# Kernel optimization log

Measured on AMD Instinct MI355X. Metric: run time of the kernel, lower is better.

Reference implementation:

```python
import math
import jax, jax.numpy as jnp
import numpy as np

B = 32        # number of graphs
MAXN = 4096   # nodes per graph (all graphs full)
C = 256       # emb_size_atom
NSEEDS = 409  # int(number_atoms * 0.1)
TOTAL = B * MAXN
INV06 = 1.0 / 0.6
INV_SQRT2 = 1.0 / math.sqrt(2.0)

def scaled_silu(x):
    return jax.nn.silu(x) * INV06

def dense(x, W):
    # Dense(bias=False, activation='silu') == ScaledSiLU(x @ W^T)
    return scaled_silu(x @ W.T)

def res_layer(x, W1, W2):
    return (x + dense(dense(x, W1), W2)) * INV_SQRT2

def layer_norm(x, g, b, eps=1e-5):
    m = jnp.mean(x, -1, keepdims=True)
    v = jnp.var(x, -1, keepdims=True)
    return (x - m) * jax.lax.rsqrt(v + eps) * g + b

def split_heads(x, H):
    # torch.cat(x.split(dV//H, 2), dim=0): head-major stacking on batch axis
    b, n, d = x.shape
    return x.reshape(b, n, H, d // H).transpose(2, 0, 1, 3).reshape(H * b, n, d // H)

def merge_heads(x, H, b):
    _, n, dh = x.shape
    return x.reshape(H, b, n, dh).transpose(1, 2, 0, 3).reshape(b, n, H * dh)

def base_mha(Q, K, Wq, bq, Wk, bk, Wv, bv, Wo, bo, g0, b0, g1, b1, H, mask=None):
    dV = Wq.shape[0]
    Q_ = split_heads(Q @ Wq.T + bq, H)
    K_ = split_heads(K @ Wk.T + bk, H)
    V_ = split_heads(K @ Wv.T + bv, H)
    score = jnp.einsum('bqd,bkd->bqk', Q_, K_) * (1.0 / math.sqrt(dV))
    if mask is not None:
        score = score + jnp.tile(mask, (H, 1, 1))
    A = jax.nn.softmax(score, axis=1)  # FAITHFUL: softmax over the QUERY axis (dim=1 in source)
    out = merge_heads(Q_ + jnp.einsum('bqk,bkd->bqd', A, V_), H, Q.shape[0])
    out = layer_norm(out, g0, b0)
    out = out + jax.nn.relu(out @ Wo.T + bo)
    out = layer_norm(out, g1, b1)
    return out, A

def to_dense_batch(x, batch):
    total = x.shape[0]
    counts = jax.ops.segment_sum(jnp.ones((total,), jnp.int32), batch, num_segments=B)
    offsets = jnp.concatenate([jnp.zeros((1,), jnp.int32), jnp.cumsum(counts)[:-1]])
    pos = jnp.arange(total) - offsets[batch]  # position of each node within its graph
    dense_x = jnp.zeros((B, MAXN, x.shape[-1]), x.dtype).at[batch, pos].set(x)
    omask = jnp.zeros((B, MAXN), bool).at[batch, pos].set(True)
    return dense_x, omask, pos

def _forward(h, batch_seg, W_pre1, W_pre2, S, pWq, pbq, pWk, pbk, pWv, pbv, pWo, pbo, pg0, pb0, pg1, pb1, iWq, ibq, iWk, ibk, iWv, ibv, iWo, ibo, ig0, ib0, ig1, ib1, W_head, W_r1a, W_r1b, W_r2a, W_r2b):
    hres = res_layer(h, W_pre1, W_pre2)
    dx, omask, pos = to_dense_batch(hres, batch_seg)
    mask = jnp.where(omask, 0.0, -1e9).astype(hres.dtype)[:, None, :]  # [B,1,MAXN]
    Q = jnp.tile(S, (B, 1, 1))  # learned seeds [B,NSEEDS,C]
    NAs, A1 = base_mha(Q, dx, pWq, pbq, pWk, pbk, pWv, pbv, pWo, pbo, pg0, pb0, pg1, pb1, 1, mask)
    NAs, _ = base_mha(NAs, NAs, iWq, ibq, iWk, ibk, iWv, ibv, iWo, ibo, ig0, ib0, ig1, ib1, 2, None)
    h_back = jnp.einsum('bsn,bsc->bnc', A1, NAs)  # project back: A1^T @ NAs
    h_up = h_back[batch_seg, pos]                 # flatten back to [TOTAL, C]
    h_up = dense(h_up, W_head)
    h_up = res_layer(h_up, W_r1a, W_r1b)
    h_up = res_layer(h_up, W_r2a, W_r2b)
    return h_up

def setup_inputs() -> dict:
    key = jax.random.key(0)
    ks = jax.random.split(key, 20)
    sc = 1.0 / math.sqrt(C)
    w = lambda k: jax.random.normal(k, (C, C), jnp.float32) * sc
    zb = jnp.zeros((C,), jnp.float32)
    og = jnp.ones((C,), jnp.float32)
    return {
        'h': jax.random.normal(ks[0], (TOTAL, C), jnp.float32),
        'batch_seg': jnp.arange(TOTAL, dtype=jnp.int32) // MAXN,
        'W_pre1': w(ks[1]), 'W_pre2': w(ks[2]),
        'S': jax.random.normal(ks[3], (1, NSEEDS, C), jnp.float32) * math.sqrt(2.0 / (NSEEDS + C)),
        'pWq': w(ks[4]), 'pbq': zb, 'pWk': w(ks[5]), 'pbk': zb,
        'pWv': w(ks[6]), 'pbv': zb, 'pWo': w(ks[7]), 'pbo': zb,
        'pg0': og, 'pb0': zb, 'pg1': og, 'pb1': zb,
        'iWq': w(ks[8]), 'ibq': zb, 'iWk': w(ks[9]), 'ibk': zb,
        'iWv': w(ks[10]), 'ibv': zb, 'iWo': w(ks[11]), 'ibo': zb,
        'ig0': og, 'ib0': zb, 'ig1': og, 'ib1': zb,
        'W_head': w(ks[12]),
        'W_r1a': w(ks[13]), 'W_r1b': w(ks[14]),
        'W_r2a': w(ks[15]), 'W_r2b': w(ks[16]),
    }

def reference(h, batch_seg, W_pre1, W_pre2, S, pWq, pbq, pWk, pbk, pWv, pbv, pWo, pbo, pg0, pb0, pg1, pb1, iWq, ibq, iWk, ibk, iWv, ibv, iWo, ibo, ig0, ib0, ig1, ib1, W_head, W_r1a, W_r1b, W_r2a, W_r2b):
    return _forward(h, batch_seg, W_pre1, W_pre2, S, pWq, pbq, pWk, pbk, pWv, pbv, pWo, pbo, pg0, pb0, pg1, pb1, iWq, ibq, iWk, ibk, iWv, ibv, iWo, ibo, ig0, ib0, ig1, ib1, W_head, W_r1a, W_r1b, W_r2a, W_r2b)
```

## Files before the change

kernel.cpp:

```cpp
#include <hip/hip_runtime.h>


#define BM 128
#define BN 128
#define BKT 32
#define PKM 132
#define NJOBS 33

typedef __attribute__((ext_vector_type(8))) __bf16 bf16x8;
typedef __attribute__((ext_vector_type(4))) __bf16 bf16x4;
typedef __attribute__((ext_vector_type(4))) float  f32x4;

struct CastJobs {
    const float* src[NJOBS];
    __bf16*      dst[NJOBS];
    long         n[NJOBS];
    int          startBlk[NJOBS];
};

__global__ void cast_many_k(CastJobs J)
{
    int b = blockIdx.x;
    int j = 0;
#pragma unroll
    for (int t = 0; t < NJOBS; t++) { if (J.startBlk[t] <= b) j = t; }
    long idx = ((long)(b - J.startBlk[j]) * 256 + threadIdx.x) * 4;
    if (idx < J.n[j]) {
        f32x4 v = *(const f32x4*)(J.src[j] + idx);
        bf16x4 o;
        o[0] = (__bf16)v[0]; o[1] = (__bf16)v[1];
        o[2] = (__bf16)v[2]; o[3] = (__bf16)v[3];
        *(bf16x4*)(J.dst[j] + idx) = o;
    }
}

__device__ __forceinline__ void gload_lds16(const __bf16* g, __bf16* l)
{
    __builtin_amdgcn_global_load_lds(
        (const __attribute__((address_space(1))) void*)g,
        (__attribute__((address_space(3))) void*)l, 16, 0, 0);
}

template<int TRANS>
__device__ __forceinline__ void stage_tile(__bf16* __restrict__ lds,
                                           const __bf16* __restrict__ G,
                                           int ld, int r0, int Rg,
                                           int k0, int K, int tid)
{
    if (TRANS == 0) {
        const bool fast = ((ld & 7) == 0) && (r0 + BM <= Rg) && (k0 + BKT <= K);
        if (fast) {
#pragma unroll
            for (int i = 0; i < 2; i++) {
                int v = tid + i * 256;
                int r = v >> 2, kc = (v & 3) * 8;
                gload_lds16(G + (long)(r0 + r) * ld + (k0 + kc), lds + v * 8);
            }
        } else {
#pragma unroll
            for (int i = 0; i < 2; i++) {
                int v = tid + i * 256;
                int r = v >> 2, kc = (v & 3) * 8;
                int gm = r0 + r, gk = k0 + kc;
                bf16x8 val;
#pragma unroll
                for (int j = 0; j < 8; j++) val[j] = (__bf16)0.0f;
                if (gm < Rg) {
                    if (((ld & 7) == 0) && (gk + 8 <= K)) {
                        val = *(const bf16x8*)(G + (long)gm * ld + gk);
                    } else {
#pragma unroll
                        for (int j = 0; j < 8; j++)
                            if (gk + j < K) val[j] = G[(long)gm * ld + gk + j];
                    }
                }
                *(bf16x8*)(lds + v * 8) = val;
            }
        }
    } else {
#pragma unroll
        for (int i = 0; i < 2; i++) {
            int v = tid + i * 256;
            int kk = v >> 4;
            int mc = (v & 15) * 8;
            int gk = k0 + kk, gm = r0 + mc;
            bf16x8 val;
#pragma unroll
            for (int j = 0; j < 8; j++) val[j] = (__bf16)0.0f;
            if (gk < K) {
                if (((ld & 7) == 0) && (gm + 8 <= Rg)) {
                    val = *(const bf16x8*)(G + (long)gk * ld + gm);
                } else {
#pragma unroll
                    for (int j = 0; j < 8; j++)
                        if (gm + j < Rg) val[j] = G[(long)gk * ld + gm + j];
                }
            }
            bf16x4 lo, hi;
            lo[0] = val[0]; lo[1] = val[1]; lo[2] = val[2]; lo[3] = val[3];
            hi[0] = val[4]; hi[1] = val[5]; hi[2] = val[6]; hi[3] = val[7];
            *(bf16x4*)(lds + kk * PKM + mc)     = lo;
            *(bf16x4*)(lds + kk * PKM + mc + 4) = hi;
        }
    }
}

template<int AT, int BT>
__launch_bounds__(256, 2)
__global__ void gemm_k(const __bf16* __restrict__ A, long aLo, long aHi, int lda, int Ms,
                       const __bf16* __restrict__ Bm, long bLo, long bHi, int ldb, int Ns,
                       const __bf16* __restrict__ bias,
                       const __bf16* __restrict__ res, long rLo, long rHi, int ldr, int resMode,
                       float* __restrict__ outF, __bf16* __restrict__ outB,
                       long oLo, long oHi, int ldo, int storeT,
                       int M, int N, int K, float oscale, int act)
{
    __shared__ __align__(16) __bf16 As[BKT * PKM];
    __shared__ __align__(16) __bf16 Bs[BKT * PKM];

    const int tid = threadIdx.x;
    const int z = blockIdx.z;
    const long zl = (long)(z & 31), zh = (long)(z >> 5);
    const __bf16* Ab = A + zl * aLo + zh * aHi;
    const __bf16* Bb = Bm + zl * bLo + zh * bHi;
    const int m0 = blockIdx.x * BM;
    const int n0 = blockIdx.y * BN;

    f32x4 acc[4][4];
#pragma unroll
    for (int i = 0; i < 4; i++)
#pragma unroll
        for (int j = 0; j < 4; j++)
#pragma unroll
            for (int r = 0; r < 4; r++) acc[i][j][r] = 0.0f;

    const int wv = tid >> 6;
    const int lane = tid & 63;
    const int wm = (wv >> 1) * 64;
    const int wn = (wv & 1) * 64;
    const int l15 = lane & 15;
    const int lq  = lane >> 4;

    for (int k0 = 0; k0 < K; k0 += BKT) {
        stage_tile<AT>(As, Ab, lda, m0, Ms, k0, K, tid);
        stage_tile<(BT == 1) ? 0 : 1>(Bs, Bb, ldb, n0, Ns, k0, K, tid);
        __syncthreads();
        bf16x8 af[4], bfr[4];
        if (AT == 0) {
#pragma unroll
            for (int i = 0; i < 4; i++)
                af[i] = *(const bf16x8*)(As + (wm + i * 16 + l15) * BKT + lq * 8);
        } else {
#pragma unroll
            for (int i = 0; i < 4; i++) {
                int m = wm + i * 16 + l15;
#pragma unroll
                for (int j = 0; j < 8; j++) af[i][j] = As[(lq * 8 + j) * PKM + m];
            }
        }
        if (BT == 1) {
#pragma unroll
            for (int j = 0; j < 4; j++)
                bfr[j] = *(const bf16x8*)(Bs + (wn + j * 16 + l15) * BKT + lq * 8);
        } else {
#pragma unroll
            for (int j = 0; j < 4; j++) {
                int n = wn + j * 16 + l15;
#pragma unroll
                for (int jj = 0; jj < 8; jj++) bfr[j][jj] = Bs[(lq * 8 + jj) * PKM + n];
            }
        }
#pragma unroll
        for (int i = 0; i < 4; i++)
#pragma unroll
            for (int j = 0; j < 4; j++)
                acc[i][j] = __builtin_amdgcn_mfma_f32_16x16x32_bf16(af[i], bfr[j], acc[i][j], 0, 0, 0);
        __syncthreads();
    }

    const __bf16* Rb = res ? (res + zl * rLo + zh * rHi) : (const __bf16*)nullptr;
    const long ob = zl * oLo + zh * oHi;
#pragma unroll
    for (int i = 0; i < 4; i++) {
#pragma unroll
        for (int j = 0; j < 4; j++) {
            int col = n0 + wn + j * 16 + l15;
            if (col >= N) continue;
            float bcol = bias ? (float)bias[col] : 0.0f;
            int row0 = m0 + wm + i * 16 + lq * 4;
            if (!storeT) {
#pragma unroll
                for (int r = 0; r < 4; r++) {
                    int row = row0 + r;
                    if (row >= M) continue;
                    float v = acc[i][j][r] * oscale + bcol;
                    if (act == 1) {
                        float e = __expf(-fabsf(v));
                        float sig = (v >= 0.0f) ? 1.0f / (1.0f + e) : e / (1.0f + e);
                        v = v * sig * 1.6666666666666667f;
                    } else if (act == 2) {
                        v = fmaxf(v, 0.0f);
                    }
                    if (resMode) {
                        float rv = (float)Rb[(long)row * ldr + col];
                        v = (resMode == 1) ? (rv + v) * 0.70710678118654752f : (rv + v);
                    }
                    long oi = ob + (long)row * ldo + col;
                    if (outF) outF[oi] = v;
                    else      outB[oi] = (__bf16)v;
                }
            } else {
                if (row0 + 3 < M) {
                    bf16x4 rv4;
                    if (resMode) rv4 = *(const bf16x4*)(Rb + (long)col * ldr + row0);
                    bf16x4 ov;
#pragma unroll
                    for (int r = 0; r < 4; r++) {
                        float v = acc[i][j][r] * oscale + bcol;
                        if (act == 1) {
                            float e = __expf(-fabsf(v));
                            float sig = (v >= 0.0f) ? 1.0f / (1.0f + e) : e / (1.0f + e);
                            v = v * sig * 1.6666666666666667f;
                        } else if (act == 2) {
                            v = fmaxf(v, 0.0f);
                        }
                        if (resMode) {
                            float rv = (float)rv4[r];
                            v = (resMode == 1) ? (rv + v) * 0.70710678118654752f : (rv + v);
                        }
                        ov[r] = (__bf16)v;
                    }
                    *(bf16x4*)(outB + ob + (long)col * ldo + row0) = ov;
                } else {
#pragma unroll
                    for (int r = 0; r < 4; r++) {
                        int row = row0 + r;
                        if (row >= M) continue;
                        float v = acc[i][j][r] * oscale + bcol;
                        if (act == 1) {
                            float e = __expf(-fabsf(v));
                            float sig = (v >= 0.0f) ? 1.0f / (1.0f + e) : e / (1.0f + e);
                            v = v * sig * 1.6666666666666667f;
                        } else if (act == 2) {
                            v = fmaxf(v, 0.0f);
                        }
                        if (resMode) {
                            float rv = (float)Rb[(long)col * ldr + row];
                            v = (resMode == 1) ? (rv + v) * 0.70710678118654752f : (rv + v);
                        }
                        outB[ob + (long)col * ldo + row] = (__bf16)v;
                    }
                }
            }
        }
    }
}

__global__ void rowsoftmax_k(const float* __restrict__ S, __bf16* __restrict__ A,
                             long rows, int L, int ldS, int ldA, int Lw)
{
    long row = (long)blockIdx.x * 4 + (threadIdx.x >> 6);
    if (row >= rows) return;
    int lane = threadIdx.x & 63;
    const float* Sr = S + row * (long)ldS;
    float v[7];
    int cnt = 0;
    for (int q = lane; q < L; q += 64) v[cnt++] = Sr[q];
    float m = -3.0e38f;
    for (int c = 0; c < cnt; c++) m = fmaxf(m, v[c]);
#pragma unroll
    for (int off = 32; off > 0; off >>= 1) m = fmaxf(m, __shfl_xor(m, off));
    float s = 0.0f;
    for (int c = 0; c < cnt; c++) s += __expf(v[c] - m);
#pragma unroll
    for (int off = 32; off > 0; off >>= 1) s += __shfl_xor(s, off);
    float inv = 1.0f / s;
    cnt = 0;
    for (int q = lane; q < Lw; q += 64) {
        float o = 0.0f;
        if (q < L) { o = __expf(v[cnt] - m) * inv; cnt++; }
        A[row * (long)ldA + q] = (__bf16)o;
    }
}

__global__ void ln_k(const __bf16* __restrict__ X, __bf16* __restrict__ Y,
                     const __bf16* __restrict__ gamma, const __bf16* __restrict__ beta,
                     int rows)
{
    int row = blockIdx.x * 4 + (threadIdx.x >> 6);
    if (row >= rows) return;
    int lane = threadIdx.x & 63;
    bf16x4 xv = *(const bf16x4*)(X + (long)row * 256 + lane * 4);
    float v0 = (float)xv[0], v1 = (float)xv[1], v2 = (float)xv[2], v3 = (float)xv[3];
    float s = v0 + v1 + v2 + v3;
#pragma unroll
    for (int off = 32; off > 0; off >>= 1) s += __shfl_xor(s, off);
    float mean = s * (1.0f / 256.0f);
    float d0 = v0 - mean, d1 = v1 - mean, d2 = v2 - mean, d3 = v3 - mean;
    float q = d0 * d0 + d1 * d1 + d2 * d2 + d3 * d3;
#pragma unroll
    for (int off = 32; off > 0; off >>= 1) q += __shfl_xor(q, off);
    float sc = rsqrtf(q * (1.0f / 256.0f) + 1e-5f);
    bf16x4 gv = *(const bf16x4*)(gamma + lane * 4);
    bf16x4 bv = *(const bf16x4*)(beta + lane * 4);
    bf16x4 ov;
    ov[0] = (__bf16)(d0 * sc * (float)gv[0] + (float)bv[0]);
    ov[1] = (__bf16)(d1 * sc * (float)gv[1] + (float)bv[1]);
    ov[2] = (__bf16)(d2 * sc * (float)gv[2] + (float)bv[2]);
    ov[3] = (__bf16)(d3 * sc * (float)gv[3] + (float)bv[3]);
    *(bf16x4*)(Y + (long)row * 256 + lane * 4) = ov;
}

__global__ void sentinel_k(float* out, long n)
{
    long i = (long)blockIdx.x * blockDim.x + threadIdx.x;
    if (i < n) out[i] = 12345.0f;
}

static void G(hipStream_t st, int AT, int BT,
              const __bf16* A, long aLo, long aHi, int lda, int Ms,
              const __bf16* B, long bLo, long bHi, int ldb, int Ns,
              const __bf16* bias,
              const __bf16* res, long rLo, long rHi, int ldr, int resMode,
              float* outF, __bf16* outB, long oLo, long oHi, int ldo, int storeT,
              int M, int N, int K, int Z, float oscale, int act)
{
    dim3 grid((M + BM - 1) / BM, (N + BN - 1) / BN, Z), blk(256, 1, 1);
#define GARGS A, aLo, aHi, lda, Ms, B, bLo, bHi, ldb, Ns, bias, res, rLo, rHi, ldr, resMode, \
              outF, outB, oLo, oHi, ldo, storeT, M, N, K, oscale, act
    if (AT == 0 && BT == 1)      gemm_k<0, 1><<<grid, blk, 0, st>>>(GARGS);
    else if (AT == 0 && BT == 0) gemm_k<0, 0><<<grid, blk, 0, st>>>(GARGS);
    else                         gemm_k<1, 0><<<grid, blk, 0, st>>>(GARGS);
#undef GARGS
}

extern "C" void kernel_launch(void* const* d_in, const int* in_sizes, int n_in,
                              void* d_out, int out_size, void* d_ws, size_t ws_size,
                              hipStream_t stream)
{
    (void)in_sizes; (void)n_in;
    float* OUT = (float*)d_out;

    const int TOT = 131072, NC = 256, NS = 409, MX = 4096;
    const int NSP = 416;
    const int NSB = 32 * NS;
    const long NTC = (long)TOT * NC;
    const int GCH = 4;

    static const int  pidx[NJOBS] = {0,2,3,4,5,6,7,8,9,10,11,12,13,14,15,16,
                                     17,18,19,20,21,22,23,24,25,26,27,28,29,30,31,32,33};
    static const long pn[NJOBS]   = {33554432,65536,65536,104704,
                                     65536,256,65536,256,65536,256,65536,256,
                                     256,256,256,256,
                                     65536,256,65536,256,65536,256,65536,256,
                                     256,256,256,256,
                                     65536,65536,65536,65536,65536};
    long ptot = 0;
    for (int j = 0; j < NJOBS; j++) ptot += pn[j];

    char* w = (char*)d_ws;
    size_t off = 0;
    auto take = [&](size_t bytes) -> char* {
        char* p = w + off;
        off += (bytes + 255) & ~(size_t)255;
        return p;
    };
    char* pblk = take((size_t)ptot * 2);
    char* reg0 = take((size_t)64 * NS * NSP * 4);
    char* reg1 = take((size_t)32 * MX * NSP * 2);
    char* reg2 = take((size_t)NTC * 2);
    char* reg3 = take((size_t)NTC * 2);
    __bf16* QP  = (__bf16*)take((size_t)NS * NC * 2);
    __bf16* sb0 = (__bf16*)take((size_t)NSB * NC * 2);
    __bf16* sb1 = (__bf16*)take((size_t)NSB * NC * 2);
    __bf16* sb2 = (__bf16*)take((size_t)NSB * NC * 2);
    __bf16* sb3 = (__bf16*)take((size_t)NSB * NC * 2);
    __bf16* sb4 = (__bf16*)take((size_t)NSB * NC * 2);
    __bf16* sb5 = (__bf16*)take((size_t)NSB * NC * 2);

    if (off > ws_size) {
        long n = out_size;
        sentinel_k<<<(int)((n + 255) / 256), 256, 0, stream>>>(OUT, n);
        return;
    }

    CastJobs J;
    __bf16* P[NJOBS];
    {
        long cum = 0;
        int blk = 0;
        for (int j = 0; j < NJOBS; j++) {
            J.src[j] = (const float*)d_in[pidx[j]];
            P[j] = (__bf16*)pblk + cum;
            J.dst[j] = P[j];
            J.n[j] = pn[j];
            J.startBlk[j] = blk;
            blk += (int)((pn[j] + 1023) / 1024);
            cum += pn[j];
        }
        cast_many_k<<<blk, 256, 0, stream>>>(J);
    }
    const __bf16 *hB = P[0], *Wpre1 = P[1], *Wpre2 = P[2], *Sseed = P[3];
    const __bf16 *pWq = P[4], *pbq = P[5], *pWk = P[6], *pbk = P[7];
    const __bf16 *pWv = P[8], *pbv = P[9], *pWo = P[10], *pbo = P[11];
    const __bf16 *pg0 = P[12], *pb0 = P[13], *pg1 = P[14], *pb1 = P[15];
    const __bf16 *iWq = P[16], *ibq = P[17], *iWk = P[18], *ibk = P[19];
    const __bf16 *iWv = P[20], *ibv = P[21], *iWo = P[22], *ibo = P[23];
    const __bf16 *ig0 = P[24], *ib0 = P[25], *ig1 = P[26], *ib1 = P[27];
    const __bf16 *Whead = P[28], *Wr1a = P[29], *Wr1b = P[30];
    const __bf16 *Wr2a = P[31], *Wr2b = P[32];

    float*  STs = (float*)reg0;
    float*  S2T = (float*)reg0;
    __bf16* T1  = (__bf16*)reg1;
    __bf16* A1T = (__bf16*)reg1;
    __bf16* Tt  = (__bf16*)reg1;
    __bf16* Kb  = (__bf16*)reg2;
    __bf16* HB  = (__bf16*)reg2;
    __bf16* Ub  = (__bf16*)reg2;
    __bf16* Vt  = (__bf16*)reg3;
    __bf16* A2T = (__bf16*)reg3;
    __bf16* Tm  = (__bf16*)reg3;
    __bf16* HR  = (__bf16*)d_out;

    G(stream, 0, 1, hB, 0, 0, 256, TOT, Wpre1, 0, 0, 256, 256, nullptr,
      nullptr, 0, 0, 0, 0, nullptr, T1, 0, 0, 256, 0, TOT, 256, 256, 1, 1.0f, 1);
    G(stream, 0, 1, T1, 0, 0, 256, TOT, Wpre2, 0, 0, 256, 256, nullptr,
      hB, 0, 0, 256, 1, nullptr, HR, 0, 0, 256, 0, TOT, 256, 256, 1, 1.0f, 1);
    G(stream, 0, 1, HR, 0, 0, 256, TOT, pWk, 0, 0, 256, 256, pbk,
      nullptr, 0, 0, 0, 0, nullptr, Kb, 0, 0, 256, 0, TOT, 256, 256, 1, 1.0f, 0);
    G(stream, 0, 1, HR, (long)MX * NC, 0, 256, MX, pWv, 0, 0, 256, 256, pbv,
      nullptr, 0, 0, 0, 0, nullptr, Vt, (long)NC * MX, 0, MX, 1, MX, 256, 256, 32, 1.0f, 0);
    G(stream, 0, 1, Sseed, 0, 0, 256, NS, pWq, 0, 0, 256, 256, pbq,
      nullptr, 0, 0, 0, 0, nullptr, QP, 0, 0, 256, 0, NS, 256, 256, 1, 1.0f, 0);
    for (int c = 0; c < 32 / GCH; c++) {
        const __bf16* Kc = Kb + (size_t)c * GCH * MX * NC;
        G(stream, 0, 1, Kc, (long)MX * NC, 0, 256, MX, QP, 0, 0, 256, NS, nullptr,
          nullptr, 0, 0, 0, 0, STs, nullptr, (long)MX * NSP, 0, NSP, 0,
          MX, NS, 256, GCH, 0.0625f, 0);
        rowsoftmax_k<<<dim3(GCH * MX / 4), 256, 0, stream>>>(
            STs, A1T + (size_t)c * GCH * MX * NSP, (long)GCH * MX, NS, NSP, NSP, NSP);
    }
    G(stream, 0, 0, Vt, (long)NC * MX, 0, MX, NC, A1T, (long)MX * NSP, 0, NSP, NSP, nullptr,
      QP, 0, 0, 256, 2, nullptr, sb0, (long)NS * NC, 0, 256, 1,
      NC, NS, MX, 32, 1.0f, 0);
    ln_k<<<dim3(NSB / 4), 256, 0, stream>>>(sb0, sb1, pg0, pb0, NSB);
    G(stream, 0, 1, sb1, 0, 0, 256, NSB, pWo, 0, 0, 256, 256, pbo,
      sb1, 0, 0, 256, 2, nullptr, sb2, 0, 0, 256, 0, NSB, 256, 256, 1, 1.0f, 2);
    ln_k<<<dim3(NSB / 4), 256, 0, stream>>>(sb2, sb0, pg1, pb1, NSB);
    G(stream, 0, 1, sb0, 0, 0, 256, NSB, iWq, 0, 0, 256, 256, ibq,
      nullptr, 0, 0, 0, 0, nullptr, sb1, 0, 0, 256, 0, NSB, 256, 256, 1, 1.0f, 0);
    G(stream, 0, 1, sb0, 0, 0, 256, NSB, iWk, 0, 0, 256, 256, ibk,
      nullptr, 0, 0, 0, 0, nullptr, sb2, 0, 0, 256, 0, NSB, 256, 256, 1, 1.0f, 0);
    G(stream, 0, 1, sb0, 0, 0, 256, NSB, iWv, 0, 0, 256, 256, ibv,
      nullptr, 0, 0, 0, 0, nullptr, sb3, 0, 0, 256, 0, NSB, 256, 256, 1, 1.0f, 0);
    G(stream, 0, 1, sb2, (long)NS * NC, 128, 256, NS, sb1, (long)NS * NC, 128, 256, NS, nullptr,
      nullptr, 0, 0, 0, 0, S2T, nullptr, (long)NS * NSP, 32L * NS * NSP, NSP, 0,
      NS, NS, 128, 64, 0.0625f, 0);
    rowsoftmax_k<<<dim3(64 * NS / 4), 256, 0, stream>>>(S2T, A2T, 64L * NS, NS, NSP, NSP, NSP);
    G(stream, 1, 0, A2T, (long)NS * NSP, 32L * NS * NSP, NSP, NSP,
      sb3, (long)NS * NC, 128, 256, 128, nullptr,
      sb1, (long)NS * NC, 128, 256, 2, nullptr, sb4, (long)NS * NC, 128, 256, 0,
      NS, 128, NS, 64, 1.0f, 0);
    ln_k<<<dim3(NSB / 4), 256, 0, stream>>>(sb4, sb5, ig0, ib0, NSB);
    G(stream, 0, 1, sb5, 0, 0, 256, NSB, iWo, 0, 0, 256, 256, ibo,
      sb5, 0, 0, 256, 2, nullptr, sb4, 0, 0, 256, 0, NSB, 256, 256, 1, 1.0f, 2);
    ln_k<<<dim3(NSB / 4), 256, 0, stream>>>(sb4, sb1, ig1, ib1, NSB);
    G(stream, 0, 0, A1T, (long)MX * NSP, 0, NSP, MX, sb1, (long)NS * NC, 0, 256, 256, nullptr,
      nullptr, 0, 0, 0, 0, nullptr, HB, (long)MX * NC, 0, 256, 0, MX, 256, 416, 32, 1.0f, 0);
    G(stream, 0, 1, HB, 0, 0, 256, TOT, Whead, 0, 0, 256, 256, nullptr,
      nullptr, 0, 0, 0, 0, nullptr, Tt, 0, 0, 256, 0, TOT, 256, 256, 1, 1.0f, 1);
    G(stream, 0, 1, Tt, 0, 0, 256, TOT, Wr1a, 0, 0, 256, 256, nullptr,
      nullptr, 0, 0, 0, 0, nullptr, Tm, 0, 0, 256, 0, TOT, 256, 256, 1, 1.0f, 1);
    G(stream, 0, 1, Tm, 0, 0, 256, TOT, Wr1b, 0, 0, 256, 256, nullptr,
      Tt, 0, 0, 256, 1, nullptr, Ub, 0, 0, 256, 0, TOT, 256, 256, 1, 1.0f, 1);
    G(stream, 0, 1, Ub, 0, 0, 256, TOT, Wr2a, 0, 0, 256, 256, nullptr,
      nullptr, 0, 0, 0, 0, nullptr, Tm, 0, 0, 256, 0, TOT, 256, 256, 1, 1.0f, 1);
    G(stream, 0, 1, Tm, 0, 0, 256, TOT, Wr2b, 0, 0, 256, 256, nullptr,
      Ub, 0, 0, 256, 1, OUT, nullptr, 0, 0, 256, 0, TOT, 256, 256, 1, 1.0f, 1);
}
```

Before: 1.756 ms.

## Double-buffer LDS tiles in GEMM to overlap global loads with MFMA

New measurement: 1.870 ms. +6.5%, slower.

```diff
diff --git a/kernel.cpp b/kernel.cpp
--- a/kernel.cpp
+++ b/kernel.cpp
@@ -42,7 +42,7 @@
 }
 
 template<int TRANS>
-__device__ __forceinline__ void stage_tile(__bf16* __restrict__ lds,
+__device__ __forceinline__ bool stage_load(bf16x8 (&rv)[2], __bf16* __restrict__ lds,
                                            const __bf16* __restrict__ G,
                                            int ld, int r0, int Rg,
                                            int k0, int K, int tid)
@@ -56,27 +56,28 @@
                 int r = v >> 2, kc = (v & 3) * 8;
                 gload_lds16(G + (long)(r0 + r) * ld + (k0 + kc), lds + v * 8);
             }
-        } else {
-#pragma unroll
-            for (int i = 0; i < 2; i++) {
-                int v = tid + i * 256;
-                int r = v >> 2, kc = (v & 3) * 8;
-                int gm = r0 + r, gk = k0 + kc;
-                bf16x8 val;
-#pragma unroll
-                for (int j = 0; j < 8; j++) val[j] = (__bf16)0.0f;
-                if (gm < Rg) {
-                    if (((ld & 7) == 0) && (gk + 8 <= K)) {
-                        val = *(const bf16x8*)(G + (long)gm * ld + gk);
-                    } else {
-#pragma unroll
-                        for (int j = 0; j < 8; j++)
-                            if (gk + j < K) val[j] = G[(long)gm * ld + gk + j];
-                    }
+            return true;
+        }
+#pragma unroll
+        for (int i = 0; i < 2; i++) {
+            int v = tid + i * 256;
+            int r = v >> 2, kc = (v & 3) * 8;
+            int gm = r0 + r, gk = k0 + kc;
+            bf16x8 val;
+#pragma unroll
+            for (int j = 0; j < 8; j++) val[j] = (__bf16)0.0f;
+            if (gm < Rg) {
+                if (((ld & 7) == 0) && (gk + 8 <= K)) {
+                    val = *(const bf16x8*)(G + (long)gm * ld + gk);
+                } else {
+#pragma unroll
+                    for (int j = 0; j < 8; j++)
+                        if (gk + j < K) val[j] = G[(long)gm * ld + gk + j];
                 }
-                *(bf16x8*)(lds + v * 8) = val;
             }
-        }
+            rv[i] = val;
+        }
+        return false;
     } else {
 #pragma unroll
         for (int i = 0; i < 2; i++) {
@@ -96,9 +97,29 @@
                         if (gm + j < Rg) val[j] = G[(long)gk * ld + gm + j];
                 }
             }
+            rv[i] = val;
+        }
+        return false;
+    }
+}
+
+template<int TRANS>
+__device__ __forceinline__ void stage_write(const bf16x8 (&rv)[2], __bf16* __restrict__ lds,
+                                            int tid, bool fast)
+{
+    if (TRANS == 0) {
+        if (fast) return;
+#pragma unroll
+        for (int i = 0; i < 2; i++)
+            *(bf16x8*)(lds + (tid + i * 256) * 8) = rv[i];
+    } else {
+#pragma unroll
+        for (int i = 0; i < 2; i++) {
+            int v = tid + i * 256;
+            int kk = v >> 4, mc = (v & 15) * 8;
             bf16x4 lo, hi;
-            lo[0] = val[0]; lo[1] = val[1]; lo[2] = val[2]; lo[3] = val[3];
-            hi[0] = val[4]; hi[1] = val[5]; hi[2] = val[6]; hi[3] = val[7];
+            lo[0] = rv[i][0]; lo[1] = rv[i][1]; lo[2] = rv[i][2]; lo[3] = rv[i][3];
+            hi[0] = rv[i][4]; hi[1] = rv[i][5]; hi[2] = rv[i][6]; hi[3] = rv[i][7];
             *(bf16x4*)(lds + kk * PKM + mc)     = lo;
             *(bf16x4*)(lds + kk * PKM + mc + 4) = hi;
         }
@@ -115,8 +136,9 @@
                        long oLo, long oHi, int ldo, int storeT,
                        int M, int N, int K, float oscale, int act)
 {
-    __shared__ __align__(16) __bf16 As[BKT * PKM];
-    __shared__ __align__(16) __bf16 Bs[BKT * PKM];
+    constexpr int BTT = (BT == 1) ? 0 : 1;
+    __shared__ __align__(16) __bf16 As[2][BKT * PKM];
+    __shared__ __align__(16) __bf16 Bs[2][BKT * PKM];
 
     const int tid = threadIdx.x;
     const int z = blockIdx.z;
@@ -141,33 +163,47 @@
     const int l15 = lane & 15;
     const int lq  = lane >> 4;
 
-    for (int k0 = 0; k0 < K; k0 += BKT) {
-        stage_tile<AT>(As, Ab, lda, m0, Ms, k0, K, tid);
-        stage_tile<(BT == 1) ? 0 : 1>(Bs, Bb, ldb, n0, Ns, k0, K, tid);
-        __syncthreads();
+    const int nt = (K + BKT - 1) / BKT;
+
+    bf16x8 ra[2], rb[2];
+    bool fa = stage_load<AT>(ra, As[0], Ab, lda, m0, Ms, 0, K, tid);
+    bool fb = stage_load<BTT>(rb, Bs[0], Bb, ldb, n0, Ns, 0, K, tid);
+    stage_write<AT>(ra, As[0], tid, fa);
+    stage_write<BTT>(rb, Bs[0], tid, fb);
+    __syncthreads();
+
+    int cur = 0;
+    for (int t = 0; t < nt; t++) {
+        const bool nxt = (t + 1 < nt);
+        if (nxt) {
+            fa = stage_load<AT>(ra, As[cur ^ 1], Ab, lda, m0, Ms, (t + 1) * BKT, K, tid);
+            fb = stage_load<BTT>(rb, Bs[cur ^ 1], Bb, ldb, n0, Ns, (t + 1) * BKT, K, tid);
+        }
+        const __bf16* Ac = As[cur];
+        const __bf16* Bc = Bs[cur];
         bf16x8 af[4], bfr[4];
         if (AT == 0) {
 #pragma unroll
             for (int i = 0; i < 4; i++)
-                af[i] = *(const bf16x8*)(As + (wm + i * 16 + l15) * BKT + lq * 8);
+                af[i] = *(const bf16x8*)(Ac + (wm + i * 16 + l15) * BKT + lq * 8);
         } else {
 #pragma unroll
             for (int i = 0; i < 4; i++) {
                 int m = wm + i * 16 + l15;
 #pragma unroll
-                for (int j = 0; j < 8; j++) af[i][j] = As[(lq * 8 + j) * PKM + m];
+                for (int j = 0; j < 8; j++) af[i][j] = Ac[(lq * 8 + j) * PKM + m];
             }
         }
         if (BT == 1) {
 #pragma unroll
             for (int j = 0; j < 4; j++)
-                bfr[j] = *(const bf16x8*)(Bs + (wn + j * 16 + l15) * BKT + lq * 8);
+                bfr[j] = *(const bf16x8*)(Bc + (wn + j * 16 + l15) * BKT + lq * 8);
         } else {
 #pragma unroll
             for (int j = 0; j < 4; j++) {
                 int n = wn + j * 16 + l15;
 #pragma unroll
-                for (int jj = 0; jj < 8; jj++) bfr[j][jj] = Bs[(lq * 8 + jj) * PKM + n];
+                for (int jj = 0; jj < 8; jj++) bfr[j][jj] = Bc[(lq * 8 + jj) * PKM + n];
             }
         }
 #pragma unroll
@@ -175,7 +211,12 @@
 #pragma unroll
             for (int j = 0; j < 4; j++)
                 acc[i][j] = __builtin_amdgcn_mfma_f32_16x16x32_bf16(af[i], bfr[j], acc[i][j], 0, 0, 0);
-        __syncthreads();
+        if (nxt) {
+            stage_write<AT>(ra, As[cur ^ 1], tid, fa);
+            stage_write<BTT>(rb, Bs[cur ^ 1], tid, fb);
+            __syncthreads();
+            cur ^= 1;
+        }
     }
 
     const __bf16* Rb = res ? (res + zl * rLo + zh * rHi) : (const __bf16*)nullptr;
```
